# Performance work log

Hardware: AMD Instinct MI355X
Metric: run time of the kernel (lower is better)

## Reference

```python
import jax, jax.numpy as jnp
import numpy as np
import math

B, L, HID = 2, 1024, 1536
NH, HD = 24, 64
DSSM = NH * HD            # 1536 (expand = 1)
QKV = 3 * DSSM
DCONV = 2
EPS = 1e-6


def _silu(u):
    return u * jax.nn.sigmoid(u)


def setup_inputs() -> dict:
    key = jax.random.key(0)
    ks = jax.random.split(key, 10)
    x = jax.random.normal(ks[0], (B, L, HID), dtype=jnp.float32)
    w_qkv = jax.random.normal(ks[1], (QKV, HID), dtype=jnp.float32) / math.sqrt(HID)
    conv_w = jax.random.normal(ks[2], (QKV, DCONV), dtype=jnp.float32) * 0.5  # depthwise causal conv, k=2
    w_dt = jax.random.normal(ks[3], (NH, HID), dtype=jnp.float32) * 0.02
    # dt_bias init exactly as in the torch module
    dt = jnp.exp(jax.random.uniform(ks[4], (NH,)) * (math.log(0.1) - math.log(0.001)) + math.log(0.001))
    dt = jnp.clip(dt, 1e-4, None)
    dt_bias = dt + jnp.log(-jnp.expm1(-dt))
    a_log = jnp.log(jax.random.uniform(ks[5], (NH,), minval=1.0, maxval=16.0))
    D = jnp.ones((NH, HD), dtype=jnp.float32)
    w_z = jax.random.normal(ks[6], (DSSM, HID), dtype=jnp.float32) / math.sqrt(HID)
    b_z = jnp.zeros((DSSM,), dtype=jnp.float32)
    rms_w = jnp.ones((DSSM,), dtype=jnp.float32)
    w_o = jax.random.normal(ks[7], (HID, DSSM), dtype=jnp.float32) / math.sqrt(DSSM)
    return dict(x=x, w_qkv=w_qkv, conv_w=conv_w, w_dt=w_dt, dt_bias=dt_bias,
                a_log=a_log, D=D, w_z=w_z, b_z=b_z, rms_w=rms_w, w_o=w_o)


def reference(x, w_qkv, conv_w, w_dt, dt_bias, a_log, D, w_z, b_z, rms_w, w_o):
    # qkv projection  [B,L,3*DSSM]
    qkv = jnp.einsum('blh,qh->blq', x, w_qkv)
    # depthwise causal conv1d (kernel size 2, padding k-1, trimmed to L)
    prev = jnp.pad(qkv, ((0, 0), (1, 0), (0, 0)))[:, :L]
    qkv = _silu(prev * conv_w[:, 0] + qkv * conv_w[:, 1])
    q, k, v = jnp.split(qkv, 3, axis=-1)
    q = q.reshape(B, L, NH, HD)
    k = k.reshape(B, L, NH, HD)
    v = v.reshape(B, L, NH, HD)
    # dt discretization: softplus(dt_proj(x) + dt_bias)   [B,L,NH]
    dt = jax.nn.softplus(jnp.einsum('blh,nh->bln', x, w_dt) + dt_bias)
    A = -jnp.exp(a_log)              # [NH], negative
    dA = dt * A                      # [B,L,NH]
    cs = jnp.transpose(jnp.cumsum(dA, axis=1), (0, 2, 1))   # [B,NH,L]
    diff = cs[:, :, :, None] - cs[:, :, None, :]            # [B,NH,L,L], <=0 on causal part
    causal = jnp.tril(jnp.ones((L, L), dtype=bool))
    decay = jnp.exp(jnp.where(causal, diff, -jnp.inf))      # segment-sum decay matrix
    # quadratic SSD (attention) form of the selective scan
    scores = jnp.einsum('bihd,bjhd->bhij', q, k) * decay
    scores = scores * jnp.transpose(dt, (0, 2, 1))[:, :, None, :]  # dt_j on keys (B-discretization)
    y = jnp.einsum('bhij,bjhd->bihd', scores, v)
    y = y + v * D                    # D skip connection
    y = y.reshape(B, L, DSSM)
    # z gate + RMSNorm + output projection
    z = jnp.einsum('blh,dh->bld', x, w_z) + b_z
    y = y * _silu(z)
    y = y * jax.lax.rsqrt(jnp.mean(y * y, axis=-1, keepdims=True) + EPS) * rms_w
    return jnp.einsum('bld,hd->blh', y, w_o)
```

## Files before the change

### kernel.cpp

```cpp
#include <hip/hip_runtime.h>
#include <hip/hip_bf16.h>
#include <math.h>

#define B_ 2
#define L_ 1024
#define HID_ 1536
#define NH_ 24
#define HD_ 64
#define DSSM_ 1536
#define QKV_ 4608
#define M_ 2048

typedef __attribute__((ext_vector_type(8))) short short8;
typedef __attribute__((ext_vector_type(4))) short short4e;
typedef __attribute__((ext_vector_type(4))) float floatx4;

__device__ __forceinline__ void gload_lds16(const short* g, short* l)
{
    __builtin_amdgcn_global_load_lds(
        (const __attribute__((address_space(1))) void*)g,
        (__attribute__((address_space(3))) void*)l,
        16, 0, 0);
}

__device__ __forceinline__ float bfs2f(short s)
{
    unsigned u = ((unsigned)(unsigned short)s) << 16;
    float f; __builtin_memcpy(&f, &u, 4); return f;
}
__device__ __forceinline__ short f2bfs(float f)
{
    __hip_bfloat16 h = __float2bfloat16(f);
    short s; __builtin_memcpy(&s, &h, 2); return s;
}

__device__ const int pIt[15] = {0,1,2,3,3,4,4,5,5,6,6,6,7,7,7};
__device__ const int pJ0[15] = {0,0,0,0,6,0,6,0,6,0,6,12,0,6,12};
__device__ const int pSl[15] = {0,0,0,0,1,0,1,0,1,0,1,2,0,1,2};

#define CN1 (QKV_ * HID_)
#define CN2 (DSSM_ * HID_)
#define CN3 (HID_ * DSSM_)

#define MFMA_ __builtin_amdgcn_mfma_f32_16x16x32_bf16
#define BAR_() __builtin_amdgcn_s_barrier()
#define SCHED_ __builtin_amdgcn_sched_barrier(0)

__global__ void cast_w_kernel(
    const float* __restrict__ wq,
    const float* __restrict__ wz, const float* __restrict__ wo,
    __hip_bfloat16* __restrict__ wcat,
    __hip_bfloat16* __restrict__ wob)
{
    int i = (blockIdx.x * 256 + threadIdx.x) * 4;
    const float* src; __hip_bfloat16* dst; int off;
    if (i < CN1)             { src = wq; dst = wcat;       off = i; }
    else if (i < CN1 + CN2)  { src = wz; dst = wcat + CN1; off = i - CN1; }
    else                     { src = wo; dst = wob;        off = i - CN1 - CN2; }
    float4 f = *reinterpret_cast<const float4*>(src + off);
    dst[off]     = __float2bfloat16(f.x);
    dst[off + 1] = __float2bfloat16(f.y);
    dst[off + 2] = __float2bfloat16(f.z);
    dst[off + 3] = __float2bfloat16(f.w);
}

__global__ __launch_bounds__(256) void dtproj_kernel(
    const float* __restrict__ x,
    const float* __restrict__ w_dt,
    const float* __restrict__ dt_bias,
    const float* __restrict__ a_log,
    float* __restrict__ dt,
    float* __restrict__ dA,
    __hip_bfloat16* __restrict__ xb)
{
    const int tid  = threadIdx.x;
    const int wave = tid >> 6;
    const int lane = tid & 63;
    const int m0   = blockIdx.x * 8 + wave * 2;

    float4 xa[2][6];
#pragma unroll
    for (int rr = 0; rr < 2; ++rr)
#pragma unroll
        for (int j = 0; j < 6; ++j)
            xa[rr][j] = *reinterpret_cast<const float4*>(
                x + (size_t)(m0 + rr) * HID_ + lane * 4 + j * 256);

    short* xbp = reinterpret_cast<short*>(xb);
#pragma unroll
    for (int rr = 0; rr < 2; ++rr)
#pragma unroll
        for (int j = 0; j < 6; ++j) {
            short4e ov;
            ov[0] = f2bfs(xa[rr][j].x); ov[1] = f2bfs(xa[rr][j].y);
            ov[2] = f2bfs(xa[rr][j].z); ov[3] = f2bfs(xa[rr][j].w);
            *reinterpret_cast<short4e*>(
                xbp + (size_t)(m0 + rr) * HID_ + lane * 4 + j * 256) = ov;
        }

    float acc0[NH_], acc1[NH_];
#pragma unroll
    for (int n = 0; n < NH_; ++n) {
        float s0 = 0.f, s1 = 0.f;
#pragma unroll
        for (int j = 0; j < 6; ++j) {
            float4 w = *reinterpret_cast<const float4*>(
                w_dt + (size_t)n * HID_ + lane * 4 + j * 256);
            s0 += xa[0][j].x * w.x + xa[0][j].y * w.y
                + xa[0][j].z * w.z + xa[0][j].w * w.w;
            s1 += xa[1][j].x * w.x + xa[1][j].y * w.y
                + xa[1][j].z * w.z + xa[1][j].w * w.w;
        }
        acc0[n] = s0;
        acc1[n] = s1;
    }

#pragma unroll
    for (int off = 32; off; off >>= 1) {
#pragma unroll
        for (int n = 0; n < NH_; ++n) {
            acc0[n] += __shfl_xor(acc0[n], off, 64);
            acc1[n] += __shfl_xor(acc1[n], off, 64);
        }
    }

    if (lane < NH_) {
        const int n = lane;
        float bias = dt_bias[n];
        float Aval = -__expf(a_log[n]);
        float v0 = acc0[n] + bias;
        float v1 = acc1[n] + bias;
        v0 = (v0 > 20.f) ? v0 : log1pf(__expf(v0));
        v1 = (v1 > 20.f) ? v1 : log1pf(__expf(v1));
        int b0 = m0 / L_, l0 = m0 % L_;
        size_t o0 = ((size_t)b0 * NH_ + n) * L_ + l0;
        dt[o0]     = v0;
        dA[o0]     = v0 * Aval;
        dt[o0 + 1] = v1;
        dA[o0 + 1] = v1 * Aval;
    }
}

#define CSTR 200

__global__ __launch_bounds__(256, 2) void gemm_qkvz_128(
    const __hip_bfloat16* __restrict__ A,
    const __hip_bfloat16* __restrict__ Bm,
    __hip_bfloat16* __restrict__ qkv_out,
    float* __restrict__ z_out,
    const float* __restrict__ b_z)
{
    extern __shared__ short lds[];
    const int K  = HID_;
    const int NT = K / 64;
    const int tid   = threadIdx.x;
    const int lane  = tid & 63;
    const int wave  = tid >> 6;
    const int col16 = lane & 15;
    const int quad  = lane >> 4;
    const int wm = wave >> 1;
    const int wn = wave & 1;
    const int rowblk = blockIdx.y * 128;
    const int colblk = blockIdx.x * 192;

    const short* Ap = reinterpret_cast<const short*>(A);
    const short* Bp = reinterpret_cast<const short*>(Bm);

    const int o  = tid * 16;
    const int s  = o ^ (((o >> 7) & 7) << 4);
    const int sr = s >> 7;
    const int sc = (s & 127) >> 1;

    const int mask = (col16 & 7) << 4;
    const int e0 = ((quad * 16)      ^ mask) >> 1;
    const int e1 = ((64 + quad * 16) ^ mask) >> 1;
    const int arow = (wm * 64 + col16) * 64;
    const int brow = (wn * 96 + col16) * 64;

    floatx4 acc[4][6] = {};

    auto STAGE_ALL = [&](int c, int t) {
        const short* ga = Ap + (size_t)(rowblk + sr) * K + t * 64 + sc;
        short* da = &lds[c * 8192 + tid * 8];
#pragma unroll
        for (int u = 0; u < 4; ++u)
            gload_lds16(ga + (size_t)(u * 32) * K, da + u * 2048);
        const short* gb = Bp + (size_t)(colblk + sr) * K + t * 64 + sc;
        short* db = &lds[16384 + c * 12288 + tid * 8];
#pragma unroll
        for (int u = 0; u < 6; ++u)
            gload_lds16(gb + (size_t)(u * 32) * K, db + u * 2048);
    };

    STAGE_ALL(0, 0);
    asm volatile("s_waitcnt vmcnt(0)" ::: "memory");
    SCHED_;
    BAR_();

    for (int t = 0; t < NT; ++t) {
        const int cur = t & 1;
        if (t + 1 < NT) STAGE_ALL(cur ^ 1, t + 1);

        const int Ab = cur * 8192;
        const int Bb = 16384 + cur * 12288;
        short8 af0[4], af1[4], bf0[6], bf1[6];
#pragma unroll
        for (int m = 0; m < 4; ++m) {
            af0[m] = *reinterpret_cast<const short8*>(&lds[Ab + arow + m * 1024 + e0]);
            af1[m] = *reinterpret_cast<const short8*>(&lds[Ab + arow + m * 1024 + e1]);
        }
#pragma unroll
        for (int n = 0; n < 6; ++n) {
            bf0[n] = *reinterpret_cast<const short8*>(&lds[Bb + brow + n * 1024 + e0]);
            bf1[n] = *reinterpret_cast<const short8*>(&lds[Bb + brow + n * 1024 + e1]);
        }
        asm volatile("s_waitcnt lgkmcnt(0)" ::: "memory");
        SCHED_;

        __builtin_amdgcn_s_setprio(1);
#pragma unroll
        for (int m = 0; m < 4; ++m)
#pragma unroll
            for (int n = 0; n < 6; ++n) {
                acc[m][n] = MFMA_(af0[m], bf0[n], acc[m][n], 0, 0, 0);
                acc[m][n] = MFMA_(af1[m], bf1[n], acc[m][n], 0, 0, 0);
            }
        __builtin_amdgcn_s_setprio(0);

        asm volatile("s_waitcnt vmcnt(0)" ::: "memory");
        SCHED_;
        BAR_();
    }

    if (blockIdx.x < 24) {
        const int rb = wm * 64 + quad * 4;
        const int cb = wn * 96 + col16;
#pragma unroll
        for (int m = 0; m < 4; ++m)
#pragma unroll
            for (int n = 0; n < 6; ++n)
#pragma unroll
                for (int r = 0; r < 4; ++r)
                    lds[(rb + m * 16 + r) * CSTR + cb + n * 16] =
                        f2bfs(acc[m][n][r]);
        __syncthreads();
        const int row = tid >> 1;
        const int seg = tid & 1;
        const short* srcp = &lds[row * CSTR + seg * 96];
        short* dstp = reinterpret_cast<short*>(qkv_out)
                    + (size_t)(rowblk + row) * QKV_ + colblk + seg * 96;
#pragma unroll
        for (int j = 0; j < 12; ++j)
            *reinterpret_cast<short8*>(dstp + j * 8) =
                *reinterpret_cast<const short8*>(srcp + j * 8);
    } else {
        const int row0  = rowblk + wm * 64;
        const int col0g = colblk + wn * 96 - QKV_;
#pragma unroll
        for (int m = 0; m < 4; ++m)
#pragma unroll
            for (int n = 0; n < 6; ++n)
#pragma unroll
                for (int r = 0; r < 4; ++r) {
                    int row = row0 + m * 16 + quad * 4 + r;
                    int col = col0g + n * 16 + col16;
                    z_out[(size_t)row * DSSM_ + col] = acc[m][n][r] + b_z[col];
                }
    }
}

template<int OUTMODE>
__global__ __launch_bounds__(256) void gemm_nt(
    const __hip_bfloat16* __restrict__ A,
    const __hip_bfloat16* __restrict__ Bm,
    void* __restrict__ Cv,
    const float* __restrict__ bias,
    int M, int N, int K)
{
    const int lane  = threadIdx.x & 63;
    const int wave  = threadIdx.x >> 6;
    const int col16 = lane & 15;
    const int quad  = lane >> 4;
    const int wr    = wave >> 1;
    const int wc    = wave & 1;
    const int rowblk = blockIdx.y * 128;
    const int colblk = blockIdx.x * 128;

    const short* Ap = reinterpret_cast<const short*>(A);
    const short* Bp = reinterpret_cast<const short*>(Bm);

    __shared__ alignas(16) short As[128 * 32];
    __shared__ alignas(16) short Bs[128 * 32];

    const int srow = lane >> 2;
    const int scol = (lane & 3) * 8;

    floatx4 acc[4][4] = {};

    for (int k0 = 0; k0 < K; k0 += 32) {
#pragma unroll
        for (int s2 = 0; s2 < 2; ++s2) {
            const int seg = wave * 2 + s2;
            gload_lds16(Ap + (size_t)(rowblk + seg * 16 + srow) * K + k0 + scol,
                        &As[seg * 512]);
            gload_lds16(Bp + (size_t)(colblk + seg * 16 + srow) * K + k0 + scol,
                        &Bs[seg * 512]);
        }
        __syncthreads();

        short8 af[4], bf[4];
#pragma unroll
        for (int t = 0; t < 4; ++t) {
            af[t] = *reinterpret_cast<const short8*>(
                &As[(wr * 64 + t * 16 + col16) * 32 + quad * 8]);
            bf[t] = *reinterpret_cast<const short8*>(
                &Bs[(wc * 64 + t * 16 + col16) * 32 + quad * 8]);
        }
#pragma unroll
        for (int mt = 0; mt < 4; ++mt)
#pragma unroll
            for (int nt = 0; nt < 4; ++nt)
                acc[mt][nt] = __builtin_amdgcn_mfma_f32_16x16x32_bf16(
                    af[mt], bf[nt], acc[mt][nt], 0, 0, 0);
        __syncthreads();
    }

    const int row0 = rowblk + wr * 64;
    const int col0 = colblk + wc * 64;
#pragma unroll
    for (int mt = 0; mt < 4; ++mt) {
#pragma unroll
        for (int nt = 0; nt < 4; ++nt) {
#pragma unroll
            for (int r = 0; r < 4; ++r) {
                int row = row0 + mt * 16 + quad * 4 + r;
                int col = col0 + nt * 16 + col16;
                float v = acc[mt][nt][r];
                if (OUTMODE == 1) v += bias[col];
                if (OUTMODE == 2)
                    ((__hip_bfloat16*)Cv)[(size_t)row * N + col] = __float2bfloat16(v);
                else
                    ((float*)Cv)[(size_t)row * N + col] = v;
            }
        }
    }
}

#define QK2 (2 * DSSM_)

__global__ __launch_bounds__(256) void convvdt_kernel(
    const __hip_bfloat16* __restrict__ raw,
    const float* __restrict__ conv_w,
    const float* __restrict__ dt,
    const float* __restrict__ dA,
    __hip_bfloat16* __restrict__ q,
    __hip_bfloat16* __restrict__ k,
    __hip_bfloat16* __restrict__ v,
    __hip_bfloat16* __restrict__ vt,
    float* __restrict__ cs)
{
    __shared__ short T[64][72];
    __shared__ float red4[4];
    const int tid = threadIdx.x;

    if (blockIdx.x >= 3840) {
        const int bnh  = blockIdx.x - 3840;
        const int lane = tid & 63;
        const int wave = tid >> 6;
        float4 dv = *reinterpret_cast<const float4*>(dA + (size_t)bnh * L_ + tid * 4);
        float s1 = dv.x + dv.y;
        float s2 = s1 + dv.z;
        float s3 = s2 + dv.w;
        float tot = s3;
        float sc = tot;
#pragma unroll
        for (int off = 1; off < 64; off <<= 1) {
            float o2 = __shfl_up(sc, off, 64);
            if (lane >= off) sc += o2;
        }
        if (lane == 63) red4[wave] = sc;
        __syncthreads();
        float woff = 0.f;
#pragma unroll
        for (int w = 0; w < 4; ++w)
            if (w < wave) woff += red4[w];
        float base = woff + sc - tot;
        float* dst = cs + (size_t)bnh * L_ + tid * 4;
        dst[0] = base + dv.x;
        dst[1] = base + s1;
        dst[2] = base + s2;
        dst[3] = base + s3;
        return;
    }

    if (blockIdx.x < 3072) {
        int idx8 = blockIdx.x * 256 + tid;
        int c8 = (idx8 % (QK2 / 8)) * 8;
        int ml = idx8 / (QK2 / 8);
        int l  = ml % L_;
        int b  = ml / L_;

        const short* base = reinterpret_cast<const short*>(raw) + (size_t)ml * QKV_ + c8;
        short8 curv = *reinterpret_cast<const short8*>(base);
        short8 prevv = {};
        if (l > 0) prevv = *reinterpret_cast<const short8*>(base - QKV_);

        float4 w0 = *reinterpret_cast<const float4*>(conv_w + c8 * 2);
        float4 w1 = *reinterpret_cast<const float4*>(conv_w + c8 * 2 + 4);
        float4 w2 = *reinterpret_cast<const float4*>(conv_w + c8 * 2 + 8);
        float4 w3 = *reinterpret_cast<const float4*>(conv_w + c8 * 2 + 12);
        const float wa[16] = {w0.x, w0.y, w0.z, w0.w, w1.x, w1.y, w1.z, w1.w,
                              w2.x, w2.y, w2.z, w2.w, w3.x, w3.y, w3.z, w3.w};

        short8 outv;
#pragma unroll
        for (int j = 0; j < 8; ++j) {
            float u = bfs2f(prevv[j]) * wa[2 * j] + bfs2f(curv[j]) * wa[2 * j + 1];
            u = fmaxf(u, -80.f);
            outv[j] = f2bfs(u / (1.f + __expf(-u)));
        }

        int part = c8 / DSSM_;
        int cc   = c8 % DSSM_;
        int nh   = cc >> 6;
        int d    = cc & 63;
        __hip_bfloat16* dst = (part == 0) ? q : k;
        *reinterpret_cast<short8*>(
            reinterpret_cast<short*>(dst) + (((size_t)b * NH_ + nh) * L_ + l) * HD_ + d)
            = outv;
        return;
    }

    const int bid2 = blockIdx.x - 3072;
    const int lt0 = (bid2 & 15) * 64;
    const int nh  = (bid2 >> 4) % NH_;
    const int b   = bid2 / (16 * NH_);
    const int bnh = b * NH_ + nh;

    {
        int row = tid >> 2;
        int cc  = (tid & 3) * 16;
        int l   = lt0 + row;
        int cglob = QK2 + nh * 64 + cc;
        const short* rp = reinterpret_cast<const short*>(raw)
                        + (size_t)(b * L_ + l) * QKV_ + cglob;
        short8 cur0 = *reinterpret_cast<const short8*>(rp);
        short8 cur1 = *reinterpret_cast<const short8*>(rp + 8);
        short8 pv0 = {}, pv1 = {};
        if (l > 0) {
            pv0 = *reinterpret_cast<const short8*>(rp - QKV_);
            pv1 = *reinterpret_cast<const short8*>(rp + 8 - QKV_);
        }
        float wa[32];
#pragma unroll
        for (int w4 = 0; w4 < 8; ++w4) {
            float4 wv = *reinterpret_cast<const float4*>(conv_w + cglob * 2 + w4 * 4);
            wa[w4 * 4]     = wv.x; wa[w4 * 4 + 1] = wv.y;
            wa[w4 * 4 + 2] = wv.z; wa[w4 * 4 + 3] = wv.w;
        }
        float dtr = dt[(size_t)bnh * L_ + l];

        short8 vo0, vo1;
#pragma unroll
        for (int j = 0; j < 8; ++j) {
            float u = bfs2f(pv0[j]) * wa[2 * j] + bfs2f(cur0[j]) * wa[2 * j + 1];
            u = fmaxf(u, -80.f);
            float sV = u / (1.f + __expf(-u));
            vo0[j] = f2bfs(sV);
            T[row][cc + j] = f2bfs(sV * dtr);

            float u2 = bfs2f(pv1[j]) * wa[16 + 2 * j] + bfs2f(cur1[j]) * wa[16 + 2 * j + 1];
            u2 = fmaxf(u2, -80.f);
            float sV2 = u2 / (1.f + __expf(-u2));
            vo1[j] = f2bfs(sV2);
            T[row][cc + 8 + j] = f2bfs(sV2 * dtr);
        }
        short* vp = reinterpret_cast<short*>(v)
                  + ((size_t)bnh * L_ + l) * HD_ + cc;
        *reinterpret_cast<short8*>(vp)     = vo0;
        *reinterpret_cast<short8*>(vp + 8) = vo1;
    }
    __syncthreads();
    {
        int d  = tid >> 2;
        int lc = (tid & 3) * 16;
        short8 o0, o1;
#pragma unroll
        for (int j = 0; j < 8; ++j) {
            o0[j] = T[lc + j][d];
            o1[j] = T[lc + 8 + j][d];
        }
        short* dst = reinterpret_cast<short*>(vt)
                   + ((size_t)bnh * HD_ + d) * L_ + lt0 + lc;
        *reinterpret_cast<short8*>(dst)     = o0;
        *reinterpret_cast<short8*>(dst + 8) = o1;
    }
}

__global__ __launch_bounds__(256) void attn_kernel(
    const __hip_bfloat16* __restrict__ q,
    const __hip_bfloat16* __restrict__ k,
    const __hip_bfloat16* __restrict__ vt,
    const float* __restrict__ cs,
    float* __restrict__ p0,
    float* __restrict__ p1,
    float* __restrict__ p2)
{
    const int bid  = blockIdx.x;
    const int xcd  = bid & 7;
    const int tq   = bid >> 3;
    const int g    = (tq / 15) * 8 + xcd;
    const int pidx = tq % 15;
    const int it   = pIt[pidx];
    const int sl   = pSl[pidx];
    const int jt_beg = pJ0[pidx];
    const int b    = g / NH_;
    const int nh   = g % NH_;
    const int tid  = threadIdx.x;
    const int lane = tid & 63;
    const int wave = tid >> 6;
    const int col  = lane & 15;
    const int quad = lane >> 4;
    const int bnh  = b * NH_ + nh;
    const int iw0  = it * 128 + wave * 16;
    const int iw1  = iw0 + 64;

    float* pout = (sl == 0) ? p0 : ((sl == 1) ? p1 : p2);

    const short* qp  = reinterpret_cast<const short*>(q);
    const short* kp  = reinterpret_cast<const short*>(k);
    const short* vtp = reinterpret_cast<const short*>(vt);

    __shared__ alignas(16) short Ks[8192];
    __shared__ alignas(16) short Ps[4 * 2 * 16 * 72];
    __shared__ float Cj[384];

    const int jbase = jt_beg * 64;
    const int jlim  = min(384, L_ - jbase);
    if (tid < (jlim >> 2))
        *reinterpret_cast<float4*>(&Cj[tid * 4]) =
            *reinterpret_cast<const float4*>(cs + (size_t)bnh * L_ + jbase + tid * 4);

    const short* qrow0 = qp + ((size_t)bnh * L_ + iw0 + col) * HD_;
    const short* qrow1 = qp + ((size_t)bnh * L_ + iw1 + col) * HD_;
    short8 aq0_0 = *reinterpret_cast<const short8*>(qrow0 + quad * 8);
    short8 aq0_1 = *reinterpret_cast<const short8*>(qrow0 + 32 + quad * 8);
    short8 aq1_0 = *reinterpret_cast<const short8*>(qrow1 + quad * 8);
    short8 aq1_1 = *reinterpret_cast<const short8*>(qrow1 + 32 + quad * 8);

    float csr0[4], csr1[4];
#pragma unroll
    for (int r = 0; r < 4; ++r) {
        csr0[r] = cs[(size_t)bnh * L_ + iw0 + quad * 4 + r];
        csr1[r] = cs[(size_t)bnh * L_ + iw1 + quad * 4 + r];
    }

    auto STAGE_K128 = [&](int t128) {
        const short* gk = kp + ((size_t)bnh * L_ + jbase + t128 * 128
                                + wave * 32 + (lane >> 2)) * HD_ + (lane & 3) * 8;
        gload_lds16(gk,                 &Ks[wave * 1024 + lane * 8]);
        gload_lds16(gk + 16 * HD_,      &Ks[wave * 1024 + 512 + lane * 8]);
        gload_lds16(gk + 32,            &Ks[4096 + wave * 1024 + lane * 8]);
        gload_lds16(gk + 16 * HD_ + 32, &Ks[4096 + wave * 1024 + 512 + lane * 8]);
    };

    const int jt_end = min(jt_beg + 5, 2 * it + 1);
    const int n128 = (jt_end - jt_beg + 1) >> 1;

    STAGE_K128(0);

    floatx4 accO0[4] = {};
    floatx4 accO1[4] = {};

    auto PROCESS = [&](int j0, int h, short8 (&bv)[2][4]) {
#pragma unroll
        for (int s = 0; s < 4; ++s) {
            int jsub = j0 + s * 16;
            short8 bk0 = *reinterpret_cast<const short8*>(
                &Ks[(h * 64 + s * 16 + col) * 32 + quad * 8]);
            short8 bk1 = *reinterpret_cast<const short8*>(
                &Ks[4096 + (h * 64 + s * 16 + col) * 32 + quad * 8]);
            int j = jsub + col;
            float csj = Cj[j - jbase];

            if (jsub <= iw0 + 15) {
                floatx4 sc = {};
                sc = __builtin_amdgcn_mfma_f32_16x16x32_bf16(aq0_0, bk0, sc, 0, 0, 0);
                sc = __builtin_amdgcn_mfma_f32_16x16x32_bf16(aq0_1, bk1, sc, 0, 0, 0);
#pragma unroll
                for (int r = 0; r < 4; ++r) {
                    int i = iw0 + quad * 4 + r;
                    float e = (j <= i) ? __expf(csr0[r] - csj) : 0.f;
                    Ps[wave * 2304 + (quad * 4 + r) * 72 + s * 16 + col] =
                        f2bfs(sc[r] * e);
                }
            } else if (j0 + (s >> 1) * 32 <= iw0 + 15) {
#pragma unroll
                for (int r = 0; r < 4; ++r)
                    Ps[wave * 2304 + (quad * 4 + r) * 72 + s * 16 + col] = 0;
            }

            if (jsub <= iw1 + 15) {
                floatx4 sc = {};
                sc = __builtin_amdgcn_mfma_f32_16x16x32_bf16(aq1_0, bk0, sc, 0, 0, 0);
                sc = __builtin_amdgcn_mfma_f32_16x16x32_bf16(aq1_1, bk1, sc, 0, 0, 0);
#pragma unroll
                for (int r = 0; r < 4; ++r) {
                    int i = iw1 + quad * 4 + r;
                    float e = (j <= i) ? __expf(csr1[r] - csj) : 0.f;
                    Ps[wave * 2304 + 1152 + (quad * 4 + r) * 72 + s * 16 + col] =
                        f2bfs(sc[r] * e);
                }
            } else if (j0 + (s >> 1) * 32 <= iw1 + 15) {
#pragma unroll
                for (int r = 0; r < 4; ++r)
                    Ps[wave * 2304 + 1152 + (quad * 4 + r) * 72 + s * 16 + col] = 0;
            }
        }

#pragma unroll
        for (int c = 0; c < 2; ++c) {
            if (j0 + c * 32 <= iw0 + 15) {
                short8 pa = *reinterpret_cast<const short8*>(
                    &Ps[wave * 2304 + col * 72 + c * 32 + quad * 8]);
#pragma unroll
                for (int nt = 0; nt < 4; ++nt)
                    accO0[nt] = __builtin_amdgcn_mfma_f32_16x16x32_bf16(
                        pa, bv[c][nt], accO0[nt], 0, 0, 0);
            }
            if (j0 + c * 32 <= iw1 + 15) {
                short8 pa = *reinterpret_cast<const short8*>(
                    &Ps[wave * 2304 + 1152 + col * 72 + c * 32 + quad * 8]);
#pragma unroll
                for (int nt = 0; nt < 4; ++nt)
                    accO1[nt] = __builtin_amdgcn_mfma_f32_16x16x32_bf16(
                        pa, bv[c][nt], accO1[nt], 0, 0, 0);
            }
        }
    };

    for (int t = 0; t < n128; ++t) {
        const int j0A = jbase + t * 128;
        const int j0B = j0A + 64;

        short8 bvA[2][4];
#pragma unroll
        for (int c = 0; c < 2; ++c) {
            if (j0A + c * 32 <= iw1 + 15) {
#pragma unroll
                for (int nt = 0; nt < 4; ++nt)
                    bvA[c][nt] = *reinterpret_cast<const short8*>(
                        vtp + ((size_t)bnh * HD_ + nt * 16 + col) * L_
                            + j0A + c * 32 + quad * 8);
            }
        }

        asm volatile("s_waitcnt vmcnt(0)" ::: "memory");
        SCHED_;
        __syncthreads();

        short8 bvB[2][4];
#pragma unroll
        for (int c = 0; c < 2; ++c) {
            if (j0B + c * 32 <= iw1 + 15) {
#pragma unroll
                for (int nt = 0; nt < 4; ++nt)
                    bvB[c][nt] = *reinterpret_cast<const short8*>(
                        vtp + ((size_t)bnh * HD_ + nt * 16 + col) * L_
                            + j0B + c * 32 + quad * 8);
            }
        }

        PROCESS(j0A, 0, bvA);
        PROCESS(j0B, 1, bvB);

        __syncthreads();
        if (t + 1 < n128) STAGE_K128(t + 1);
    }

#pragma unroll
    for (int nt = 0; nt < 4; ++nt) {
#pragma unroll
        for (int r = 0; r < 4; ++r) {
            int dv = nt * 16 + col;
            int i0 = iw0 + quad * 4 + r;
            int i1 = iw1 + quad * 4 + r;
            pout[((size_t)b * L_ + i0) * DSSM_ + nh * HD_ + dv] = accO0[nt][r];
            pout[((size_t)b * L_ + i1) * DSSM_ + nh * HD_ + dv] = accO1[nt][r];
        }
    }
}

__global__ __launch_bounds__(256) void gate_rms_kernel(
    const float* __restrict__ p0,
    const float* __restrict__ p1,
    const float* __restrict__ p2,
    const float* __restrict__ z,
    const __hip_bfloat16* __restrict__ v,
    const float* __restrict__ Dm,
    const float* __restrict__ rms_w,
    __hip_bfloat16* __restrict__ yn)
{
    int m   = blockIdx.x;
    int b   = m / L_;
    int l   = m % L_;
    int tid = threadIdx.x;
    size_t base = (size_t)m * DSSM_;
    const bool has1 = (l >= 384);
    const bool has2 = (l >= 768);

    floatx4 acc4[2] = {};
    float ss = 0.f;
#pragma unroll
    for (int t = 0; t < 2; ++t) {
        int i4 = t * 256 + tid;
        if (i4 < DSSM_ / 4) {
            int c  = i4 * 4;
            int nh = c >> 6, d = c & 63;
            floatx4 p = *reinterpret_cast<const floatx4*>(p0 + base + c);
            if (has1) p += *reinterpret_cast<const floatx4*>(p1 + base + c);
            if (has2) p += *reinterpret_cast<const floatx4*>(p2 + base + c);
            floatx4 dm = *reinterpret_cast<const floatx4*>(Dm + c);
            floatx4 zz = *reinterpret_cast<const floatx4*>(z + base + c);
            short4e vv = *reinterpret_cast<const short4e*>(
                reinterpret_cast<const short*>(v)
                + (((size_t)b * NH_ + nh) * L_ + l) * HD_ + d);
            floatx4 g;
#pragma unroll
            for (int j = 0; j < 4; ++j) {
                float yv = p[j] + bfs2f(vv[j]) * dm[j];
                float zv = fmaxf(zz[j], -80.f);
                float gv = yv * (zv / (1.f + __expf(-zv)));
                ss += gv * gv;
                g[j] = gv;
            }
            acc4[t] = g;
        }
    }
#pragma unroll
    for (int off = 32; off; off >>= 1) ss += __shfl_xor(ss, off, 64);
    __shared__ float red[4];
    if ((tid & 63) == 0) red[tid >> 6] = ss;
    __syncthreads();
    ss = red[0] + red[1] + red[2] + red[3];
    float r = rsqrtf(ss / (float)DSSM_ + 1e-6f);
#pragma unroll
    for (int t = 0; t < 2; ++t) {
        int i4 = t * 256 + tid;
        if (i4 < DSSM_ / 4) {
            int c = i4 * 4;
            floatx4 rw = *reinterpret_cast<const floatx4*>(rms_w + c);
            short4e o;
#pragma unroll
            for (int j = 0; j < 4; ++j)
                o[j] = f2bfs(acc4[t][j] * r * rw[j]);
            *reinterpret_cast<short4e*>(
                reinterpret_cast<short*>(yn) + base + c) = o;
        }
    }
}

extern "C" void kernel_launch(void* const* d_in, const int* in_sizes, int n_in,
                              void* d_out, int out_size, void* d_ws, size_t ws_size,
                              hipStream_t stream)
{
    const float* x       = (const float*)d_in[0];
    const float* w_qkv   = (const float*)d_in[1];
    const float* conv_w  = (const float*)d_in[2];
    const float* w_dt    = (const float*)d_in[3];
    const float* dt_bias = (const float*)d_in[4];
    const float* a_log   = (const float*)d_in[5];
    const float* Dm      = (const float*)d_in[6];
    const float* w_z     = (const float*)d_in[7];
    const float* b_z     = (const float*)d_in[8];
    const float* rms_w   = (const float*)d_in[9];
    const float* w_o     = (const float*)d_in[10];
    float* out = (float*)d_out;

    char* ws = (char*)d_ws;

    __hip_bfloat16* xb    = (__hip_bfloat16*)(ws);
    __hip_bfloat16* wob   = (__hip_bfloat16*)(ws + 6291456);
    float*          zbuf  = (float*)(ws + 11010048);
    __hip_bfloat16* wcat  = (__hip_bfloat16*)(ws + 23592960);
    __hip_bfloat16* qkvb  = (__hip_bfloat16*)(ws + 42467328);
    __hip_bfloat16* qb    = (__hip_bfloat16*)(ws + 61341696);
    __hip_bfloat16* kb    = (__hip_bfloat16*)(ws + 67633152);
    __hip_bfloat16* vb    = (__hip_bfloat16*)(ws + 73924608);
    float* dt   = (float*)(ws + 80216064);
    float* dA   = (float*)(ws + 80412672);
    float* cs   = (float*)(ws + 80609280);
    __hip_bfloat16* vtb = (__hip_bfloat16*)(ws);
    __hip_bfloat16* yn  = (__hip_bfloat16*)(ws);
    float* p0 = (float*)(ws + 23592960);
    float* p1 = (float*)(ws + 36175872);
    float* p2 = (float*)(ws + 48758784);

    static bool attr_set = false;
    if (!attr_set) {
        (void)hipFuncSetAttribute(reinterpret_cast<const void*>(gemm_qkvz_128),
                                  hipFuncAttributeMaxDynamicSharedMemorySize,
                                  81920);
        attr_set = true;
    }

    cast_w_kernel<<<(CN1 + CN2 + CN3) / 1024, 256, 0, stream>>>(
        w_qkv, w_z, w_o, wcat, wob);

    dtproj_kernel<<<M_ / 8, 256, 0, stream>>>(
        x, w_dt, dt_bias, a_log, dt, dA, xb);

    gemm_qkvz_128<<<dim3((QKV_ + DSSM_) / 192, M_ / 128), 256, 81920, stream>>>(
        xb, wcat, qkvb, zbuf, b_z);

    convvdt_kernel<<<3888, 256, 0, stream>>>(
        qkvb, conv_w, dt, dA, qb, kb, vb, vtb, cs);

    attn_kernel<<<720, 256, 0, stream>>>(
        qb, kb, vtb, cs, p0, p1, p2);

    gate_rms_kernel<<<M_, 256, 0, stream>>>(p0, p1, p2, zbuf, vb, Dm, rms_w, yn);

    gemm_nt<0><<<dim3(HID_ / 128, M_ / 128), 256, 0, stream>>>(
        yn, wob, (void*)out, nullptr, M_, HID_, DSSM_);
}
```

Baseline: 253.4 us.

## Replace output GEMM with double-buffered swizzled 128x96 tile kernel

Replaces the generic single-buffered 128x128 output-projection GEMM with a specialized kernel that uses K-tile 64, double-buffered LDS staging via direct global-to-LDS loads, XOR-swizzled LDS layout to avoid bank conflicts, and 128x96 tiles. The 96-wide tile raises the grid from 192 to 256 blocks to better fill the CUs, and prefetching the next tile overlaps memory with MFMA work. It uses more dynamic LDS (57 KB) and more register pressure per block.

Measured after the change: 239.1 us. 1.06x faster.

```diff
diff --git a/kernel.cpp b/kernel.cpp
--- a/kernel.cpp
+++ b/kernel.cpp
@@ -269,81 +269,105 @@
     }
 }
 
-template<int OUTMODE>
-__global__ __launch_bounds__(256) void gemm_nt(
+__global__ __launch_bounds__(256, 2) void gemm_out_128(
     const __hip_bfloat16* __restrict__ A,
     const __hip_bfloat16* __restrict__ Bm,
-    void* __restrict__ Cv,
-    const float* __restrict__ bias,
-    int M, int N, int K)
-{
-    const int lane  = threadIdx.x & 63;
-    const int wave  = threadIdx.x >> 6;
+    float* __restrict__ Co)
+{
+    extern __shared__ short lds[];
+    const int K  = DSSM_;
+    const int NT = K / 64;
+    const int tid   = threadIdx.x;
+    const int lane  = tid & 63;
+    const int wave  = tid >> 6;
     const int col16 = lane & 15;
     const int quad  = lane >> 4;
-    const int wr    = wave >> 1;
-    const int wc    = wave & 1;
+    const int wm = wave >> 1;
+    const int wn = wave & 1;
     const int rowblk = blockIdx.y * 128;
-    const int colblk = blockIdx.x * 128;
+    const int colblk = blockIdx.x * 96;
 
     const short* Ap = reinterpret_cast<const short*>(A);
     const short* Bp = reinterpret_cast<const short*>(Bm);
 
-    __shared__ alignas(16) short As[128 * 32];
-    __shared__ alignas(16) short Bs[128 * 32];
-
-    const int srow = lane >> 2;
-    const int scol = (lane & 3) * 8;
-
-    floatx4 acc[4][4] = {};
-
-    for (int k0 = 0; k0 < K; k0 += 32) {
-#pragma unroll
-        for (int s2 = 0; s2 < 2; ++s2) {
-            const int seg = wave * 2 + s2;
-            gload_lds16(Ap + (size_t)(rowblk + seg * 16 + srow) * K + k0 + scol,
-                        &As[seg * 512]);
-            gload_lds16(Bp + (size_t)(colblk + seg * 16 + srow) * K + k0 + scol,
-                        &Bs[seg * 512]);
-        }
-        __syncthreads();
-
-        short8 af[4], bf[4];
-#pragma unroll
-        for (int t = 0; t < 4; ++t) {
-            af[t] = *reinterpret_cast<const short8*>(
-                &As[(wr * 64 + t * 16 + col16) * 32 + quad * 8]);
-            bf[t] = *reinterpret_cast<const short8*>(
-                &Bs[(wc * 64 + t * 16 + col16) * 32 + quad * 8]);
-        }
-#pragma unroll
-        for (int mt = 0; mt < 4; ++mt)
-#pragma unroll
-            for (int nt = 0; nt < 4; ++nt)
-                acc[mt][nt] = __builtin_amdgcn_mfma_f32_16x16x32_bf16(
-                    af[mt], bf[nt], acc[mt][nt], 0, 0, 0);
-        __syncthreads();
-    }
-
-    const int row0 = rowblk + wr * 64;
-    const int col0 = colblk + wc * 64;
-#pragma unroll
-    for (int mt = 0; mt < 4; ++mt) {
-#pragma unroll
-        for (int nt = 0; nt < 4; ++nt) {
+    const int o  = tid * 16;
+    const int s  = o ^ (((o >> 7) & 7) << 4);
+    const int sr = s >> 7;
+    const int sc = (s & 127) >> 1;
+
+    const int mask = (col16 & 7) << 4;
+    const int e0 = ((quad * 16)      ^ mask) >> 1;
+    const int e1 = ((64 + quad * 16) ^ mask) >> 1;
+    const int arow = (wm * 64 + col16) * 64;
+    const int brow = (wn * 48 + col16) * 64;
+
+    floatx4 acc[4][3] = {};
+
+    auto STAGE_ALL = [&](int c, int t) {
+        const short* ga = Ap + (size_t)(rowblk + sr) * K + t * 64 + sc;
+        short* da = &lds[c * 8192 + tid * 8];
+#pragma unroll
+        for (int u = 0; u < 4; ++u)
+            gload_lds16(ga + (size_t)(u * 32) * K, da + u * 2048);
+        const short* gb = Bp + (size_t)(colblk + sr) * K + t * 64 + sc;
+        short* db = &lds[16384 + c * 6144 + tid * 8];
+#pragma unroll
+        for (int u = 0; u < 3; ++u)
+            gload_lds16(gb + (size_t)(u * 32) * K, db + u * 2048);
+    };
+
+    STAGE_ALL(0, 0);
+    asm volatile("s_waitcnt vmcnt(0)" ::: "memory");
+    SCHED_;
+    BAR_();
+
+    for (int t = 0; t < NT; ++t) {
+        const int cur = t & 1;
+        if (t + 1 < NT) STAGE_ALL(cur ^ 1, t + 1);
+
+        const int Ab = cur * 8192;
+        const int Bb = 16384 + cur * 6144;
+        short8 af0[4], af1[4], bf0[3], bf1[3];
+#pragma unroll
+        for (int m = 0; m < 4; ++m) {
+            af0[m] = *reinterpret_cast<const short8*>(&lds[Ab + arow + m * 1024 + e0]);
+            af1[m] = *reinterpret_cast<const short8*>(&lds[Ab + arow + m * 1024 + e1]);
+        }
+#pragma unroll
+        for (int n = 0; n < 3; ++n) {
+            bf0[n] = *reinterpret_cast<const short8*>(&lds[Bb + brow + n * 1024 + e0]);
+            bf1[n] = *reinterpret_cast<const short8*>(&lds[Bb + brow + n * 1024 + e1]);
+        }
+        asm volatile("s_waitcnt lgkmcnt(0)" ::: "memory");
+        SCHED_;
+
+        __builtin_amdgcn_s_setprio(1);
+#pragma unroll
+        for (int m = 0; m < 4; ++m)
+#pragma unroll
+            for (int n = 0; n < 3; ++n) {
+                acc[m][n] = MFMA_(af0[m], bf0[n], acc[m][n], 0, 0, 0);
+                acc[m][n] = MFMA_(af1[m], bf1[n], acc[m][n], 0, 0, 0);
+            }
+        __builtin_amdgcn_s_setprio(0);
+
+        asm volatile("s_waitcnt vmcnt(0)" ::: "memory");
+        SCHED_;
+        BAR_();
+    }
+
+    const int row0 = rowblk + wm * 64;
+    const int col0 = colblk + wn * 48;
+#pragma unroll
+    for (int m = 0; m < 4; ++m)
+#pragma unroll
+        for (int n = 0; n < 3; ++n)
 #pragma unroll
             for (int r = 0; r < 4; ++r) {
-                int row = row0 + mt * 16 + quad * 4 + r;
-                int col = col0 + nt * 16 + col16;
-                float v = acc[mt][nt][r];
-                if (OUTMODE == 1) v += bias[col];
-                if (OUTMODE == 2)
-                    ((__hip_bfloat16*)Cv)[(size_t)row * N + col] = __float2bfloat16(v);
-                else
-                    ((float*)Cv)[(size_t)row * N + col] = v;
-            }
-        }
-    }
+                int row = row0 + m * 16 + quad * 4 + r;
+                int col = col0 + n * 16 + col16;
+                Co[(size_t)row * HID_ + col] = acc[m][n][r];
+            }
 }
 
 #define QK2 (2 * DSSM_)
@@ -801,6 +825,9 @@
         (void)hipFuncSetAttribute(reinterpret_cast<const void*>(gemm_qkvz_128),
                                   hipFuncAttributeMaxDynamicSharedMemorySize,
                                   81920);
+        (void)hipFuncSetAttribute(reinterpret_cast<const void*>(gemm_out_128),
+                                  hipFuncAttributeMaxDynamicSharedMemorySize,
+                                  57344);
         attr_set = true;
     }
 
@@ -821,6 +848,6 @@
 
     gate_rms_kernel<<<M_, 256, 0, stream>>>(p0, p1, p2, zbuf, vb, Dm, rms_w, yn);
 
-    gemm_nt<0><<<dim3(HID_ / 128, M_ / 128), 256, 0, stream>>>(
-        yn, wob, (void*)out, nullptr, M_, HID_, DSSM_);
-}
+    gemm_out_128<<<dim3(HID_ / 96, M_ / 128), 256, 57344, stream>>>(
+        yn, wob, out);
+}
```
